# Kernel optimization log

Measured on AMD Instinct MI355X. Metric: run time of the kernel, lower is better.

Reference implementation:

```python
import jax, jax.numpy as jnp
import numpy as np

DIM = 1024
NUM_HEADS = 16
HEAD_DIM = 64
NUM_LANDMARKS = 256
SEQ_LEN = 4096
BATCH = 4


def setup_inputs() -> dict:
    key = jax.random.key(0)
    ks = jax.random.split(key, 10)
    hd = NUM_HEADS * HEAD_DIM
    s = 1.0 / np.sqrt(DIM)
    inp = {
        "X": jax.random.normal(ks[0], (BATCH, SEQ_LEN, DIM), jnp.float32),
        "mask": jnp.ones((BATCH, SEQ_LEN), jnp.float32),
        "Wq": jax.random.normal(ks[1], (DIM, hd), jnp.float32) * s,
        "bq": jnp.zeros((hd,), jnp.float32),
        "Wk": jax.random.normal(ks[2], (DIM, hd), jnp.float32) * s,
        "bk": jnp.zeros((hd,), jnp.float32),
        "Wv": jax.random.normal(ks[3], (DIM, hd), jnp.float32) * s,
        "bv": jnp.zeros((hd,), jnp.float32),
        "Wff": jax.random.normal(ks[4], (hd, DIM), jnp.float32) * (1.0 / np.sqrt(hd)),
        "bff": jnp.zeros((DIM,), jnp.float32),
    }
    return inp


def _iterative_inv(mat, n_iter=6):
    # mat: [B,H,m,m]; Newton-Schulz style pseudo-inverse, faithful to torch code
    m = mat.shape[-1]
    I = jnp.eye(m, dtype=mat.dtype)
    K = mat
    # global max over the whole tensor, as torch.max with no dim
    denom = jnp.max(jnp.sum(jnp.abs(K), axis=-2)) * jnp.max(jnp.sum(jnp.abs(K), axis=-1))
    V = jnp.swapaxes(K, -1, -2) / denom
    for _ in range(n_iter):
        KV = K @ V
        V = 0.25 * V @ (13.0 * I - KV @ (15.0 * I - KV @ (7.0 * I - KV)))
    return V


def _nystrom_attn(Q, K, V, mask):
    # Q,K,V: [B,H,S,D]; mask: [B,S]
    B, H, S, D = Q.shape
    m = NUM_LANDMARKS
    scale = np.sqrt(np.sqrt(HEAD_DIM)).astype(np.float32)
    Q = Q * mask[:, None, :, None] / scale
    K = K * mask[:, None, :, None] / scale
    Ql = Q.reshape(B, H, m, S // m, D).mean(axis=-2)  # [B,H,m,D]
    Kl = K.reshape(B, H, m, S // m, D).mean(axis=-2)
    k1 = jax.nn.softmax(jnp.einsum('bhsd,bhmd->bhsm', Q, Kl), axis=-1)   # [B,H,S,m]
    k2 = jax.nn.softmax(jnp.einsum('bhmd,bhnd->bhmn', Ql, Kl), axis=-1)  # [B,H,m,m]
    k3 = jax.nn.softmax(
        jnp.einsum('bhmd,bhsd->bhms', Ql, K) - 1e9 * (1.0 - mask[:, None, None, :]),
        axis=-1)  # [B,H,m,S]
    return k1 @ (_iterative_inv(k2) @ (k3 @ V))  # [B,H,S,D]


def reference(X, mask, Wq, bq, Wk, bk, Wv, bv, Wff, bff):
    B, S, _ = X.shape
    def split(t):  # [B,S,H*D] -> [B,H,S,D]
        return t.reshape(B, S, NUM_HEADS, HEAD_DIM).transpose(0, 2, 1, 3)
    Q = split(X @ Wq + bq)
    K = split(X @ Wk + bk)
    V = split(X @ Wv + bv)
    attn = _nystrom_attn(Q, K, V, mask)
    attn = attn.transpose(0, 2, 1, 3).reshape(B, S, NUM_HEADS * HEAD_DIM)
    return attn @ Wff + bff
```

## Files before the change

kernel.cpp:

```cpp
#include <hip/hip_runtime.h>
#include <cstdint>
#include <cstddef>


typedef unsigned short u16;
typedef __attribute__((ext_vector_type(8))) short short8;
typedef __attribute__((ext_vector_type(4))) float f32x4;
typedef __attribute__((ext_vector_type(4))) unsigned short us4;
typedef __attribute__((ext_vector_type(8))) unsigned short us8;

__device__ __forceinline__ float bf2f(u16 u){ return __uint_as_float(((unsigned int)u)<<16); }
__device__ __forceinline__ u16 f2bf(float x){
  unsigned int i = __float_as_uint(x);
  unsigned int r = i + 0x7FFFu + ((i>>16)&1u);
  return (u16)(r>>16);
}
__device__ __forceinline__ f32x4 mfma16(short8 a, short8 b, f32x4 c){
  return __builtin_amdgcn_mfma_f32_16x16x32_bf16(a,b,c,0,0,0);
}
__device__ __forceinline__ void gld16(const void* g, void* l){
  __builtin_amdgcn_global_load_lds(
      (const __attribute__((address_space(1))) unsigned int*)g,
      (__attribute__((address_space(3))) unsigned int*)l, 16, 0, 0);
}

template<typename T>
__device__ __forceinline__ void load4v(const T* p, float x[4]){
  if constexpr (sizeof(T)==4){
    f32x4 v = *(const f32x4*)p;
    #pragma unroll
    for (int c=0;c<4;c++) x[c]=v[c];
  } else {
    us4 v = *(const us4*)p;
    #pragma unroll
    for (int c=0;c<4;c++) x[c]=bf2f(v[c]);
  }
}

template<int BM,int BN,int AM,int AN,bool BTB,bool SPLIT,bool FUSESM,
         typename TA,typename TB,typename TC>
__global__ __launch_bounds__(256) void gemm_k(
    const TA* __restrict__ A, const TB* __restrict__ B, TC* __restrict__ C,
    int M, int N, int K,
    long long sA, long long sB, long long sC, int ldc)
{
  constexpr int WR = BM/(16*AM);
  constexpr int WC = BN/(16*AN);
  static_assert(WR*WC==4, "need 4 waves");
  constexpr int LDW = 40;
  constexpr int NROW = BM+BN;
  constexpr int LOFF = NROW*LDW;
  __shared__ u16 lds[(SPLIT?2:1)*NROW*LDW];

  const int tid = threadIdx.x;
  const int z = blockIdx.z;
  const TA* __restrict__ Az = A + (size_t)z*sA;
  const TB* __restrict__ Bz = B + (size_t)z*sB;
  TC* __restrict__ Cz = C + (size_t)z*sC;
  const int tileM = blockIdx.x*BM;
  const int tileN = blockIdx.y*BN;

  const int lane = tid & 63;
  const int wv   = tid >> 6;
  const int wr   = wv / WC;
  const int wc   = wv % WC;
  const int lrow = lane & 15;
  const int kgrp = lane >> 4;
  const int koff = kgrp*8;

  f32x4 acc[AM][AN];
  #pragma unroll
  for (int i=0;i<AM;i++)
    #pragma unroll
    for (int j=0;j<AN;j++)
      acc[i][j] = (f32x4){0.f,0.f,0.f,0.f};

  u16* ldsA = lds;
  u16* ldsB = lds + BM*LDW;

  const int nkt = K >> 5;
  for (int kt=0; kt<nkt; ++kt){
    const int k0 = kt << 5;
    #pragma unroll
    for (int s2=0; s2<BM/32; ++s2){
      int slot = tid + s2*256;
      int row = slot >> 3;
      int kc  = (slot & 7) << 2;
      float x[4];
      load4v(Az + (size_t)(tileM+row)*K + (k0+kc), x);
      us4 h, l;
      #pragma unroll
      for (int c=0;c<4;c++){
        h[c] = f2bf(x[c]);
        if constexpr (SPLIT) l[c] = f2bf(x[c] - bf2f(h[c]));
      }
      *(us4*)&ldsA[row*LDW + kc] = h;
      if constexpr (SPLIT) *(us4*)&ldsA[LOFF + row*LDW + kc] = l;
    }
    {
      #pragma unroll
      for (int s2=0; s2<BN/32; ++s2){
        int slot = tid + s2*256;
        int row = slot >> 3;
        int kc  = (slot & 7) << 2;
        float x[4];
        load4v(Bz + (size_t)(tileN+row)*K + (k0+kc), x);
        us4 h, l;
        #pragma unroll
        for (int c=0;c<4;c++){
          h[c] = f2bf(x[c]);
          if constexpr (SPLIT) l[c] = f2bf(x[c] - bf2f(h[c]));
        }
        *(us4*)&ldsB[row*LDW + kc] = h;
        if constexpr (SPLIT) *(us4*)&ldsB[LOFF + row*LDW + kc] = l;
      }
    }
    __syncthreads();
    short8 ah[AM], al[AM];
    #pragma unroll
    for (int i=0;i<AM;i++){
      ah[i] = *(const short8*)&ldsA[(wr*AM*16 + i*16 + lrow)*LDW + koff];
      if constexpr (SPLIT) al[i] = *(const short8*)&ldsA[LOFF + (wr*AM*16 + i*16 + lrow)*LDW + koff];
    }
    #pragma unroll
    for (int j=0;j<AN;j++){
      short8 bh = *(const short8*)&ldsB[(wc*AN*16 + j*16 + lrow)*LDW + koff];
      if constexpr (SPLIT){
        short8 bl = *(const short8*)&ldsB[LOFF + (wc*AN*16 + j*16 + lrow)*LDW + koff];
        #pragma unroll
        for (int i=0;i<AM;i++){
          acc[i][j] = mfma16(ah[i], bh, acc[i][j]);
          acc[i][j] = mfma16(ah[i], bl, acc[i][j]);
          acc[i][j] = mfma16(al[i], bh, acc[i][j]);
        }
      } else {
        #pragma unroll
        for (int i=0;i<AM;i++)
          acc[i][j] = mfma16(ah[i], bh, acc[i][j]);
      }
    }
    __syncthreads();
  }

  #pragma unroll
  for (int r=0;r<4;r++){
    float mx = -3.0e38f;
    #pragma unroll
    for (int j=0;j<AN;j++) mx = fmaxf(mx, acc[0][j][r]);
    #pragma unroll
    for (int d=1; d<16; d<<=1) mx = fmaxf(mx, __shfl_xor(mx, d));
    float p[AN]; float ss = 0.f;
    #pragma unroll
    for (int j=0;j<AN;j++){ p[j] = expf(acc[0][j][r]-mx); ss += p[j]; }
    #pragma unroll
    for (int d=1; d<16; d<<=1) ss += __shfl_xor(ss, d);
    float inv = 1.0f/ss;
    int row = tileM + wr*16 + kgrp*4 + r;
    #pragma unroll
    for (int j=0;j<AN;j++){
      int col = j*16 + lrow;
      Cz[(size_t)row*ldc + col] = p[j]*inv;
    }
  }
}

template<int OUT>
__global__ __launch_bounds__(256) void sgemm_k(
    const u16* __restrict__ Ah, const u16* __restrict__ Al,
    const u16* __restrict__ Bh, const u16* __restrict__ Bl,
    int K, long long sA, long long sB,
    u16* __restrict__ RoH, u16* __restrict__ RoL,
    u16* __restrict__ CoH, u16* __restrict__ CoL,
    float* __restrict__ Fo, long long sO, int ldO,
    float addI, float csgn, float scale,
    const float* __restrict__ bias, const float* __restrict__ ml)
{
  __shared__ u16 lds[16384];
  const int tid = threadIdx.x;
  const int z = blockIdx.z;
  const int tileM = blockIdx.x*64, tileN = blockIdx.y*64;
  const int lane = tid&63, wv = tid>>6;
  const int wr = wv>>1, wc = wv&1;
  const int lrow = lane&15, kgrp = lane>>4;

  const u16* __restrict__ base[4] = {
    Ah + (size_t)z*sA + (size_t)tileM*K,
    Al + (size_t)z*sA + (size_t)tileM*K,
    Bh + (size_t)z*sB + (size_t)tileN*K,
    Bl + (size_t)z*sB + (size_t)tileN*K };

  f32x4 acc[2][2];
  #pragma unroll
  for (int i=0;i<2;i++)
    #pragma unroll
    for (int j=0;j<2;j++) acc[i][j] = (f32x4){0.f,0.f,0.f,0.f};

  for (int k0=0; k0<K; k0+=64){
    #pragma unroll
    for (int t4=0; t4<4; ++t4){
      #pragma unroll
      for (int hf=0; hf<2; ++hf){
        int w = hf*256 + tid;
        int row = w>>3, c = w&7;
        int cs = c ^ (row&7);
        gld16(base[t4] + (size_t)row*K + k0 + cs*8, lds + t4*4096 + (w & ~63)*8);
      }
    }
    __syncthreads();
    #pragma unroll
    for (int kk=0; kk<2; ++kk){
      int ch = kk*4 + kgrp;
      short8 a_h[2], a_l[2], b_h[2], b_l[2];
      #pragma unroll
      for (int i=0;i<2;i++){
        int r = wr*32 + i*16 + lrow;
        int off = r*64 + ((ch ^ (r&7))<<3);
        a_h[i] = *(const short8*)&lds[off];
        a_l[i] = *(const short8*)&lds[4096 + off];
      }
      #pragma unroll
      for (int j=0;j<2;j++){
        int r = wc*32 + j*16 + lrow;
        int off = r*64 + ((ch ^ (r&7))<<3);
        b_h[j] = *(const short8*)&lds[8192 + off];
        b_l[j] = *(const short8*)&lds[12288 + off];
      }
      #pragma unroll
      for (int i=0;i<2;i++)
        #pragma unroll
        for (int j=0;j<2;j++){
          acc[i][j] = mfma16(a_h[i], b_h[j], acc[i][j]);
          acc[i][j] = mfma16(a_h[i], b_l[j], acc[i][j]);
          acc[i][j] = mfma16(a_l[i], b_h[j], acc[i][j]);
        }
    }
    __syncthreads();
  }

  if constexpr (OUT==0 || OUT==1){
    #pragma unroll
    for (int i=0;i<2;i++)
      #pragma unroll
      for (int j=0;j<2;j++){
        int rl0 = wr*32 + i*16 + kgrp*4;
        int cl  = wc*32 + j*16 + lrow;
        #pragma unroll
        for (int q=0;q<4;q++){
          int rl = rl0 + q;
          float p = acc[i][j][q]*scale;
          if constexpr (OUT==0){
            if (RoH){
              u16 h = f2bf(p);
              int lo = rl*64 + (cl ^ ((rl&7)<<3));
              lds[lo] = h;
              lds[4096 + lo] = f2bf(p - bf2f(h));
            }
            float cv = csgn*p + (((tileM+rl)==(tileN+cl))? addI : 0.f);
            u16 ch = f2bf(cv);
            int lo2 = cl*64 + (rl ^ ((cl&7)<<3));
            lds[8192 + lo2] = ch;
            lds[12288 + lo2] = f2bf(cv - bf2f(ch));
          } else {
            lds[cl*64 + (rl ^ ((cl&7)<<3))] = f2bf(p);
          }
        }
      }
    __syncthreads();
    if constexpr (OUT==0){
      if (RoH){
        #pragma unroll
        for (int c2=0;c2<2;c2++){
          int idx = c2*256 + tid;
          int row = idx>>3, seg = idx&7;
          int lo = row*64 + ((seg ^ (row&7))<<3);
          size_t go = (size_t)z*65536 + (size_t)(tileM+row)*256 + tileN + seg*8;
          *(us8*)&RoH[go] = *(const us8*)&lds[lo];
          *(us8*)&RoL[go] = *(const us8*)&lds[4096 + lo];
        }
      }
      #pragma unroll
      for (int c2=0;c2<2;c2++){
        int idx = c2*256 + tid;
        int row = idx>>3, seg = idx&7;
        int lo = row*64 + ((seg ^ (row&7))<<3);
        size_t go = (size_t)z*65536 + (size_t)(tileN+row)*256 + tileM + seg*8;
        *(us8*)&CoH[go] = *(const us8*)&lds[8192 + lo];
        *(us8*)&CoL[go] = *(const us8*)&lds[12288 + lo];
      }
    } else {
      #pragma unroll
      for (int c2=0;c2<2;c2++){
        int idx = c2*256 + tid;
        int row = idx>>3, seg = idx&7;
        int lo = row*64 + ((seg ^ (row&7))<<3);
        *(us8*)&CoH[(size_t)z*16384 + (size_t)(tileN+row)*256 + tileM + seg*8] =
            *(const us8*)&lds[lo];
      }
    }
  } else {
    #pragma unroll
    for (int i=0;i<2;i++)
      #pragma unroll
      for (int j=0;j<2;j++){
        int grow0 = tileM + wr*32 + i*16 + kgrp*4;
        int gcol  = tileN + wc*32 + j*16 + lrow;
        #pragma unroll
        for (int q=0;q<4;q++){
          int grow = grow0+q;
          float v = acc[i][j][q] + ml[grow]*bias[gcol];
          int b = grow>>8, l = grow&255, h = gcol>>6, d = gcol&63;
          size_t oi = (((size_t)(b*16+h)*256 + l)*64 + d);
          Fo[oi] = v;
          if (RoH) RoH[oi] = f2bf(v);
        }
      }
  }
}

template<int EPI>
__global__ __launch_bounds__(256) void fgemm_k(
    const u16* __restrict__ A, const u16* __restrict__ Bt, float* __restrict__ Cf,
    u16* __restrict__ Q_, u16* __restrict__ K_, u16* __restrict__ V_,
    int M, int N, int K, int nTilesN,
    const float* __restrict__ bias, const float* __restrict__ rowscale)
{
  __shared__ u16 lds[2*128*64];
  u16* ldsA = lds;
  u16* ldsB = lds + 128*64;

  int flat = blockIdx.y*nTilesN + blockIdx.x;
  int nwg  = gridDim.x*gridDim.y;
  int chunk = nwg >> 3;
  int nid = (flat & 7)*chunk + (flat >> 3);
  int bxM = nid / nTilesN, byN = nid % nTilesN;
  const int tileM = bxM*128, tileN = byN*128;

  const int tid = threadIdx.x;
  const int lane = tid & 63, wv = tid>>6;
  const int wr = wv>>1, wc = wv&1;
  const int lrow = lane&15, kgrp = lane>>4;

  f32x4 acc[4][4];
  #pragma unroll
  for (int i=0;i<4;i++)
    #pragma unroll
    for (int j=0;j<4;j++) acc[i][j] = (f32x4){0.f,0.f,0.f,0.f};

  for (int k0=0; k0<K; k0+=64){
    #pragma unroll
    for (int i=0;i<4;i++){
      int s = i*256 + tid;
      int row = s>>3, c = s&7;
      int cs = c ^ (row&7);
      gld16(A + (size_t)(tileM+row)*K + k0 + cs*8, ldsA + (size_t)(s & ~63)*8);
    }
    #pragma unroll
    for (int i=0;i<4;i++){
      int s = i*256 + tid;
      int row = s>>3, c = s&7;
      int cs = c ^ (row&7);
      gld16(Bt + (size_t)(tileN+row)*K + k0 + cs*8, ldsB + (size_t)(s & ~63)*8);
    }
    __syncthreads();
    #pragma unroll
    for (int kk=0; kk<2; ++kk){
      int ch = kk*4 + kgrp;
      short8 af[4], bf[4];
      #pragma unroll
      for (int i=0;i<4;i++){
        int r = wr*64 + i*16 + lrow;
        af[i] = *(const short8*)&ldsA[r*64 + ((ch^(r&7))<<3)];
      }
      #pragma unroll
      for (int j=0;j<4;j++){
        int r = wc*64 + j*16 + lrow;
        bf[j] = *(const short8*)&ldsB[r*64 + ((ch^(r&7))<<3)];
      }
      #pragma unroll
      for (int i=0;i<4;i++)
        #pragma unroll
        for (int j=0;j<4;j++)
          acc[i][j] = mfma16(af[i], bf[j], acc[i][j]);
    }
    __syncthreads();
  }

  if constexpr (EPI==0){
    #pragma unroll
    for (int i=0;i<4;i++)
      #pragma unroll
      for (int j=0;j<4;j++)
        #pragma unroll
        for (int q=0;q<4;q++){
          int row = tileM + wr*64 + i*16 + kgrp*4 + q;
          int col = tileN + wc*64 + j*16 + lrow;
          Cf[(size_t)row*N + col] = acc[i][j][q] + (bias ? bias[col] : 0.f);
        }
  } else {
    #pragma unroll
    for (int i=0;i<4;i++)
      #pragma unroll
      for (int j=0;j<4;j++)
        #pragma unroll
        for (int q=0;q<4;q++){
          int rloc = wr*64 + i*16 + kgrp*4 + q;
          int cloc = wc*64 + j*16 + lrow;
          int col = tileN + cloc;
          float v = acc[i][j][q] + bias[col];
          if ((col>>10) < 2) v *= rowscale[tileM + rloc];
          lds[rloc*128 + cloc] = f2bf(v);
        }
    __syncthreads();
    #pragma unroll
    for (int c=0;c<8;c++){
      int idx = c*256 + tid;
      int row = idx >> 4;
      int seg = idx & 15;
      int col = tileN + seg*8;
      int which = col >> 10;
      int hd = col & 1023, h = hd>>6, d0 = hd&63;
      int grow = tileM + row;
      int b = grow>>12, s = grow&4095;
      u16* dst = (which==0) ? Q_ : (which==1) ? K_ : V_;
      us8 v = *(const us8*)&lds[row*128 + seg*8];
      *(us8*)&dst[(((size_t)(b*16+h))*4096 + s)*64 + d0] = v;
    }
  }
}

__global__ __launch_bounds__(256) void o3p_k(
    const float* __restrict__ Ql, const u16* __restrict__ Kb, const u16* __restrict__ Vb,
    const float* __restrict__ mask, float* __restrict__ Opart, float* __restrict__ MLpart)
{
  constexpr int QHI=0, QLO=4096, KT=8192, VT=12288, PHI=16640, PLO=20736;
  __shared__ u16 lds[24832];
  const int bx = blockIdx.x, ck = blockIdx.y, z = blockIdx.z;
  const int tid = threadIdx.x;
  const int lane = tid&63, wv = tid>>6;
  const int lrow = lane&15, kgrp = lane>>4;
  const float* Qlz = Ql + (size_t)z*16384 + (size_t)bx*64*64;
  const u16* Kz = Kb + (size_t)z*4096*64;
  const u16* Vz = Vb + (size_t)z*4096*64;
  const float* mrow = mask + (size_t)(z>>4)*4096;

  #pragma unroll
  for (int i=0;i<2;i++){
    int s = i*256 + tid;
    int row = s>>3, c = s&7;
    const float* src = Qlz + row*64 + c*8;
    f32x4 v0 = *(const f32x4*)src;
    f32x4 v1 = *(const f32x4*)(src+4);
    us8 hi, lo;
    #pragma unroll
    for (int e=0;e<4;e++){
      hi[e] = f2bf(v0[e]); lo[e] = f2bf(v0[e]-bf2f(hi[e]));
      hi[4+e] = f2bf(v1[e]); lo[4+e] = f2bf(v1[e]-bf2f(hi[4+e]));
    }
    int ad = row*64 + ((c^(row&7))<<3);
    *(us8*)&lds[QHI+ad] = hi;
    *(us8*)&lds[QLO+ad] = lo;
  }

  float m_r[4], l_r[4];
  f32x4 oacc[4];
  #pragma unroll
  for (int r=0;r<4;r++){ m_r[r] = -3.0e38f; l_r[r] = 0.f; }
  #pragma unroll
  for (int j=0;j<4;j++) oacc[j] = (f32x4){0.f,0.f,0.f,0.f};

  for (int st=0; st<16; ++st){
    int s0 = (ck*16 + st)*64;
    #pragma unroll
    for (int i=0;i<2;i++){
      int s = i*256 + tid;
      int row = s>>3, c = s&7;
      int cs = c ^ (row&7);
      gld16(Kz + (size_t)(s0+row)*64 + cs*8, &lds[KT + (size_t)(s & ~63)*8]);
    }
    #pragma unroll
    for (int i=0;i<2;i++){
      int s = i*256 + tid;
      int row = s>>3, c = s&7;
      us8 v = *(const us8*)(Vz + (size_t)(s0+row)*64 + c*8);
      #pragma unroll
      for (int e=0;e<8;e++) lds[VT + (c*8+e)*68 + row] = v[e];
    }
    __syncthreads();

    f32x4 sacc[4];
    #pragma unroll
    for (int j=0;j<4;j++) sacc[j] = (f32x4){0.f,0.f,0.f,0.f};
    int qr = wv*16 + lrow;
    #pragma unroll
    for (int kk=0; kk<2; ++kk){
      int ch = kk*4 + kgrp;
      short8 ah = *(const short8*)&lds[QHI + qr*64 + ((ch^(qr&7))<<3)];
      short8 alo = *(const short8*)&lds[QLO + qr*64 + ((ch^(qr&7))<<3)];
      #pragma unroll
      for (int j=0;j<4;j++){
        int kr = j*16 + lrow;
        short8 bk = *(const short8*)&lds[KT + kr*64 + ((ch^(kr&7))<<3)];
        sacc[j] = mfma16(ah, bk, sacc[j]);
        sacc[j] = mfma16(alo, bk, sacc[j]);
      }
    }
    float mb[4];
    #pragma unroll
    for (int j=0;j<4;j++) mb[j] = -1.0e9f*(1.0f - mrow[s0 + j*16 + lrow]);
    #pragma unroll
    for (int j=0;j<4;j++)
      #pragma unroll
      for (int r=0;r<4;r++) sacc[j][r] += mb[j];

    #pragma unroll
    for (int r=0;r<4;r++){
      float tm = fmaxf(fmaxf(sacc[0][r],sacc[1][r]), fmaxf(sacc[2][r],sacc[3][r]));
      #pragma unroll
      for (int d=1; d<16; d<<=1) tm = fmaxf(tm, __shfl_xor(tm, d));
      float mn = fmaxf(m_r[r], tm);
      float scf = expf(m_r[r] - mn);
      float ps[4]; float tsum = 0.f;
      #pragma unroll
      for (int j=0;j<4;j++){ ps[j] = expf(sacc[j][r] - mn); tsum += ps[j]; }
      #pragma unroll
      for (int d=1; d<16; d<<=1) tsum += __shfl_xor(tsum, d);
      l_r[r] = l_r[r]*scf + tsum;
      m_r[r] = mn;
      #pragma unroll
      for (int j=0;j<4;j++) oacc[j][r] *= scf;
      int prow = kgrp*4 + r;
      #pragma unroll
      for (int j=0;j<4;j++){
        int key = j*16 + lrow;
        u16 phi = f2bf(ps[j]);
        u16 plo = f2bf(ps[j] - bf2f(phi));
        int ad = wv*1024 + prow*64 + (((key>>3)^(prow&7))<<3) + (key&7);
        lds[PHI+ad] = phi;
        lds[PLO+ad] = plo;
      }
    }

    #pragma unroll
    for (int kk=0; kk<2; ++kk){
      int ch = kk*4 + kgrp;
      int pr = lrow;
      short8 pah = *(const short8*)&lds[PHI + wv*1024 + pr*64 + ((ch^(pr&7))<<3)];
      short8 plo = *(const short8*)&lds[PLO + wv*1024 + pr*64 + ((ch^(pr&7))<<3)];
      #pragma unroll
      for (int j=0;j<4;j++){
        int vr = j*16 + lrow;
        int a0 = VT + vr*68 + ch*8;
        us4 p0 = *(const us4*)&lds[a0];
        us4 p1 = *(const us4*)&lds[a0+4];
        short8 bv_;
        #pragma unroll
        for (int e=0;e<4;e++){ bv_[e] = (short)p0[e]; bv_[4+e] = (short)p1[e]; }
        oacc[j] = mfma16(pah, bv_, oacc[j]);
        oacc[j] = mfma16(plo, bv_, oacc[j]);
      }
    }
    __syncthreads();
  }

  #pragma unroll
  for (int j=0;j<4;j++)
    #pragma unroll
    for (int r=0;r<4;r++){
      int rowl = bx*64 + wv*16 + kgrp*4 + r;
      Opart[(((size_t)(ck*64+z)*256 + rowl)*64) + j*16 + lrow] = oacc[j][r];
    }
  #pragma unroll
  for (int r=0;r<4;r++){
    if (lrow==0){
      int rowl = bx*64 + wv*16 + kgrp*4 + r;
      MLpart[((size_t)(ck*64+z)*256 + rowl)*2 + 0] = m_r[r];
      MLpart[((size_t)(ck*64+z)*256 + rowl)*2 + 1] = l_r[r];
    }
  }
}

__global__ __launch_bounds__(256) void o3c_k(const float* __restrict__ Opart,
    const float* __restrict__ MLpart, u16* __restrict__ O3Th, u16* __restrict__ O3Tl)
{
  int z = blockIdx.x; int t = threadIdx.x;
  float m[4], l[4];
  #pragma unroll
  for (int c=0;c<4;c++){
    m[c] = MLpart[((size_t)(c*64+z)*256 + t)*2 + 0];
    l[c] = MLpart[((size_t)(c*64+z)*256 + t)*2 + 1];
  }
  float M = fmaxf(fmaxf(m[0],m[1]), fmaxf(m[2],m[3]));
  float w[4]; float L = 0.f;
  #pragma unroll
  for (int c=0;c<4;c++){ w[c] = expf(m[c]-M); L += l[c]*w[c]; }
  float inv = 1.0f/L;
  for (int d0=0; d0<16; ++d0){
    f32x4 o = (f32x4){0.f,0.f,0.f,0.f};
    #pragma unroll
    for (int c=0;c<4;c++){
      f32x4 x = *(const f32x4*)(Opart + ((size_t)(c*64+z)*256 + t)*64 + d0*4);
      #pragma unroll
      for (int e=0;e<4;e++) o[e] += w[c]*x[e];
    }
    #pragma unroll
    for (int e=0;e<4;e++){
      float val = o[e]*inv;
      int d = d0*4+e;
      u16 h = f2bf(val);
      O3Th[((size_t)z*64 + d)*256 + t] = h;
      O3Tl[((size_t)z*64 + d)*256 + t] = f2bf(val - bf2f(h));
    }
  }
}

__global__ void fill_k(float* __restrict__ p, int n, float v){
  for (int i = blockIdx.x*256 + threadIdx.x; i < n; i += gridDim.x*256) p[i] = v;
}
__global__ void prep_k(const float* __restrict__ mask, float* __restrict__ rs,
                       const float* __restrict__ bq, const float* __restrict__ bk,
                       const float* __restrict__ bv, float* __restrict__ bqkv,
                       float* __restrict__ mx){
  int b = blockIdx.x;
  if (b < 64){
    int i = b*256 + threadIdx.x;
    rs[i] = mask[i] * 0.3535533905932738f;
  } else if (b < 76){
    int j = (b-64)*256 + threadIdx.x;
    bqkv[j] = (j<1024) ? bq[j] : (j<2048) ? bk[j-1024] : bv[j-2048];
  } else {
    if (threadIdx.x < 2) mx[threadIdx.x] = 0.f;
  }
}
__global__ __launch_bounds__(256) void wtr4_k(
    const float* __restrict__ Wq, const float* __restrict__ Wk,
    const float* __restrict__ Wv, const float* __restrict__ Wff,
    u16* __restrict__ Tqkv, u16* __restrict__ Tff){
  __shared__ float t[64][65];
  int zi = blockIdx.z;
  const float* W = (zi==0)?Wq:(zi==1)?Wk:(zi==2)?Wv:Wff;
  u16* T = (zi==3)? Tff : (Tqkv + (size_t)zi*1048576);
  int ti = blockIdx.x, tj = blockIdx.y;
  int tt = threadIdx.x; int c = tt&63, r0 = tt>>6;
  #pragma unroll
  for (int rr=0; rr<16; rr++){
    int r = rr*4 + r0;
    t[r][c] = W[(size_t)(ti*64+r)*1024 + tj*64 + c];
  }
  __syncthreads();
  #pragma unroll
  for (int rr=0; rr<16; rr++){
    int r = rr*4 + r0;
    T[(size_t)(tj*64 + r)*1024 + ti*64 + c] = f2bf(t[c][r]);
  }
}
__global__ __launch_bounds__(256) void wtrsplit2_k(
    const float* __restrict__ Wq, const float* __restrict__ Wk,
    u16* __restrict__ QH, u16* __restrict__ QL,
    u16* __restrict__ KH, u16* __restrict__ KL){
  __shared__ float t[64][65];
  int zi = blockIdx.z;
  const float* W = zi ? Wk : Wq;
  u16* TH = zi ? KH : QH;
  u16* TL = zi ? KL : QL;
  int ti = blockIdx.x, tj = blockIdx.y;
  int tt = threadIdx.x; int c = tt&63, r0 = tt>>6;
  #pragma unroll
  for (int rr=0; rr<16; rr++){
    int r = rr*4 + r0;
    t[r][c] = W[(size_t)(ti*64+r)*1024 + tj*64 + c];
  }
  __syncthreads();
  #pragma unroll
  for (int rr=0; rr<16; rr++){
    int r = rr*4 + r0;
    float v = t[c][r];
    u16 h = f2bf(v);
    TH[(size_t)(tj*64 + r)*1024 + ti*64 + c] = h;
    TL[(size_t)(tj*64 + r)*1024 + ti*64 + c] = f2bf(v - bf2f(h));
  }
}
__global__ __launch_bounds__(256) void pool_k(const float* __restrict__ X, const float* __restrict__ mask,
                                              u16* __restrict__ Xlh, u16* __restrict__ Xll,
                                              float* __restrict__ ml, u16* __restrict__ Xb){
  int bl = blockIdx.x; int b = bl>>8; int l = bl&255;
  const float* Xp = X + ((size_t)b*4096 + (size_t)l*16)*1024;
  const float* mp = mask + (size_t)b*4096 + (size_t)l*16;
  int t = threadIdx.x;
  f32x4 acc = (f32x4){0.f,0.f,0.f,0.f};
  float msum = 0.f;
  #pragma unroll
  for (int j=0;j<16;j++){
    float mj = mp[j];
    msum += mj;
    f32x4 x = *(const f32x4*)(Xp + (size_t)j*1024 + t*4);
    us4 xb;
    #pragma unroll
    for (int c=0;c<4;c++){ acc[c] += mj*x[c]; xb[c] = f2bf(x[c]); }
    *(us4*)(Xb + ((size_t)bl*16 + j)*1024 + t*4) = xb;
  }
  const float c0 = 0.02209708691207961f;
  us4 h, lo;
  #pragma unroll
  for (int c=0;c<4;c++){
    float v = acc[c]*c0;
    h[c] = f2bf(v);
    lo[c] = f2bf(v - bf2f(h[c]));
  }
  *(us4*)(Xlh + (size_t)bl*1024 + t*4) = h;
  *(us4*)(Xll + (size_t)bl*1024 + t*4) = lo;
  if (t==0) ml[bl] = msum * c0;
}
__global__ __launch_bounds__(256) void absmax_k(const float* __restrict__ k2, float* __restrict__ mx){
  int z = blockIdx.x; int t = threadIdx.x;
  const float* A = k2 + (size_t)z*65536;
  float rsum=0.f, csum=0.f;
  for (int j=0;j<256;j++){
    rsum += fabsf(A[t*256+j]);
    csum += fabsf(A[j*256+t]);
  }
  #pragma unroll
  for (int d=1; d<64; d<<=1){
    rsum = fmaxf(rsum, __shfl_xor(rsum, d));
    csum = fmaxf(csum, __shfl_xor(csum, d));
  }
  __shared__ float red[8];
  int wv=t>>6, ln=t&63;
  if (ln==0){ red[wv]=rsum; red[4+wv]=csum; }
  __syncthreads();
  if (t==0){
    float mr = fmaxf(fmaxf(red[0],red[1]),fmaxf(red[2],red[3]));
    float mc = fmaxf(fmaxf(red[4],red[5]),fmaxf(red[6],red[7]));
    atomicMax((int*)&mx[0], __float_as_int(mr));
    atomicMax((int*)&mx[1], __float_as_int(mc));
  }
}
__global__ __launch_bounds__(256) void v0prep_k(const float* __restrict__ K2f, const float* __restrict__ mx,
    u16* __restrict__ K2h, u16* __restrict__ K2l,
    u16* __restrict__ V0rh, u16* __restrict__ V0rl,
    u16* __restrict__ V0ch, u16* __restrict__ V0cl)
{
  int z = blockIdx.y; int bx = blockIdx.x;
  int ti = bx>>2, tj = bx&3;
  __shared__ float tile[64][65];
  const float* A = K2f + (size_t)z*65536;
  int t = threadIdx.x; int c = t&63, r0 = t>>6;
  float invden = 1.0f/(mx[0]*mx[1]);
  #pragma unroll
  for (int rr=0; rr<16; rr++){
    int r = rr*4 + r0;
    float v = A[(size_t)(ti*64 + r)*256 + tj*64 + c];
    tile[r][c] = v;
    size_t idx = (size_t)z*65536 + (size_t)(ti*64+r)*256 + tj*64 + c;
    u16 h = f2bf(v);
    K2h[idx] = h; K2l[idx] = f2bf(v - bf2f(h));
    float w = v*invden;
    h = f2bf(w);
    V0ch[idx] = h; V0cl[idx] = f2bf(w - bf2f(h));
  }
  __syncthreads();
  #pragma unroll
  for (int rr=0; rr<16; rr++){
    int r = rr*4 + r0;
    float w = tile[c][r]*invden;
    size_t idx = (size_t)z*65536 + (size_t)(tj*64+r)*256 + ti*64 + c;
    u16 h = f2bf(w);
    V0rh[idx] = h; V0rl[idx] = f2bf(w - bf2f(h));
  }
}

__device__ __forceinline__ int swz64(int row,int k){
  return row*64 + (((((k>>3)&7) ^ (row&7)))<<3) + (k&7);
}
__device__ __forceinline__ int swz256(int row,int k){
  return row*256 + ((((k>>3) ^ (row&7)))<<3) + (k&7);
}
__global__ __launch_bounds__(256) void attn_k(const u16* __restrict__ Qb,
    const u16* __restrict__ Klb, const u16* __restrict__ tTb,
    u16* __restrict__ attn){
  __shared__ u16 lds[32768];
  const int z = blockIdx.y;
  const int rows0 = blockIdx.x * 64;
  const int tid = threadIdx.x;
  const int lane = tid & 63, wv = tid>>6;
  const int lrow = lane & 15, kgrp = lane>>4;
  const u16* Qz = Qb + ((size_t)z*4096 + rows0)*64;
  const u16* Klz = Klb + (size_t)z*16384;
  const u16* tTz = tTb + (size_t)z*16384;

  #pragma unroll
  for (int i=0;i<8;i++){
    int s = i*256 + tid;
    int row = s>>3, c = s&7;
    gld16(Klz + (size_t)row*64 + ((c^(row&7))<<3), lds + (s & ~63)*8);
  }
  #pragma unroll
  for (int i=0;i<2;i++){
    int s = i*256 + tid;
    int row = s>>3, c = s&7;
    gld16(Qz + (size_t)row*64 + ((c^(row&7))<<3), lds + 16384 + (s & ~63)*8);
  }
  __syncthreads();

  f32x4 acc[4][4];
  #pragma unroll
  for (int i=0;i<4;i++)
    #pragma unroll
    for (int j=0;j<4;j++) acc[i][j] = (f32x4){0.f,0.f,0.f,0.f};
  #pragma unroll
  for (int ks=0; ks<2; ++ks){
    int ko = ks*32 + kgrp*8;
    short8 a[4], b[4];
    #pragma unroll
    for (int i=0;i<4;i++) a[i] = *(const short8*)&lds[16384 + swz64(16*i+lrow, ko)];
    #pragma unroll
    for (int j=0;j<4;j++) b[j] = *(const short8*)&lds[swz64(wv*64 + j*16 + lrow, ko)];
    #pragma unroll
    for (int i=0;i<4;i++)
      #pragma unroll
      for (int j=0;j<4;j++) acc[i][j] = mfma16(a[i], b[j], acc[i][j]);
  }
  __syncthreads();

  #pragma unroll
  for (int i=0;i<8;i++){
    int s = i*256 + tid;
    int row = s>>5, c = s&31;
    int gch = (c & ~7) | ((c ^ row) & 7);
    gld16(tTz + (size_t)row*256 + (gch<<3), lds + 16384 + (s & ~63)*8);
  }

  float* r0 = (float*)lds;
  float* r1 = r0 + 256;
  #pragma unroll
  for (int i=0;i<4;i++)
    #pragma unroll
    for (int r=0;r<4;r++){
      float mx = fmaxf(fmaxf(acc[i][0][r], acc[i][1][r]), fmaxf(acc[i][2][r], acc[i][3][r]));
      #pragma unroll
      for (int d=1; d<16; d<<=1) mx = fmaxf(mx, __shfl_xor(mx, d));
      if (lrow==0) r0[(16*i + kgrp*4 + r)*4 + wv] = mx;
    }
  __syncthreads();
  float inv_ir[4][4];
  #pragma unroll
  for (int i=0;i<4;i++)
    #pragma unroll
    for (int r=0;r<4;r++){
      int row = 16*i + kgrp*4 + r;
      float gm = fmaxf(fmaxf(r0[row*4+0], r0[row*4+1]), fmaxf(r0[row*4+2], r0[row*4+3]));
      float s = 0.f;
      #pragma unroll
      for (int j=0;j<4;j++){
        acc[i][j][r] = expf(acc[i][j][r] - gm);
        s += acc[i][j][r];
      }
      #pragma unroll
      for (int d=1; d<16; d<<=1) s += __shfl_xor(s, d);
      if (lrow==0) r1[row*4 + wv] = s;
      inv_ir[i][r] = 0.f; (void)inv_ir;
    }
  __syncthreads();
  #pragma unroll
  for (int i=0;i<4;i++)
    #pragma unroll
    for (int r=0;r<4;r++){
      int row = 16*i + kgrp*4 + r;
      inv_ir[i][r] = 1.0f/(r1[row*4+0]+r1[row*4+1]+r1[row*4+2]+r1[row*4+3]);
    }
  __syncthreads();

  #pragma unroll
  for (int i=0;i<4;i++)
    #pragma unroll
    for (int j=0;j<4;j++)
      #pragma unroll
      for (int r=0;r<4;r++){
        int row = 16*i + kgrp*4 + r;
        int l = wv*64 + j*16 + lrow;
        lds[swz256(row, l)] = f2bf(acc[i][j][r]*inv_ir[i][r]);
      }
  __syncthreads();

  f32x4 o[4];
  #pragma unroll
  for (int j=0;j<4;j++) o[j] = (f32x4){0.f,0.f,0.f,0.f};
  #pragma unroll
  for (int ks=0; ks<8; ++ks){
    int ko = ks*32 + kgrp*8;
    short8 a = *(const short8*)&lds[swz256(16*wv + lrow, ko)];
    #pragma unroll
    for (int j=0;j<4;j++){
      short8 bb = *(const short8*)&lds[16384 + swz256(j*16 + lrow, ko)];
      o[j] = mfma16(a, bb, o[j]);
    }
  }
  __syncthreads();
  #pragma unroll
  for (int j=0;j<4;j++)
    #pragma unroll
    for (int r=0;r<4;r++){
      int m = 16*wv + kgrp*4 + r;
      lds[m*64 + j*16 + lrow] = f2bf(o[j][r]);
    }
  __syncthreads();
  int b = z>>4, h = z&15;
  #pragma unroll
  for (int c=0;c<2;c++){
    int idx = c*256 + tid;
    int row = idx >> 3;
    int seg = idx & 7;
    us8 v = *(const us8*)&lds[row*64 + seg*8];
    *(us8*)&attn[((size_t)b*4096 + rows0 + row)*1024 + (size_t)h*64 + seg*8] = v;
  }
}

extern "C" void kernel_launch(void* const* d_in, const int* in_sizes, int n_in,
                              void* d_out, int out_size, void* d_ws, size_t ws_size,
                              hipStream_t stream) {
  (void)in_sizes; (void)n_in;
  const float* X    = (const float*)d_in[0];
  const float* mask = (const float*)d_in[1];
  const float* Wq   = (const float*)d_in[2];
  const float* bq   = (const float*)d_in[3];
  const float* Wk   = (const float*)d_in[4];
  const float* bk   = (const float*)d_in[5];
  const float* Wv   = (const float*)d_in[6];
  const float* bv   = (const float*)d_in[7];
  const float* Wff  = (const float*)d_in[8];
  const float* bff  = (const float*)d_in[9];
  float* outp = (float*)d_out;
  char* ws = (char*)d_ws;

  auto MiB = [](size_t x){ return x<<20; };
  const size_t O_QB   = 0;
  const size_t O_KB   = MiB(32);
  const size_t O_VB   = MiB(64);
  const size_t O_XB   = MiB(96);
  const size_t O_RG[4][2] = {
    {MiB(32),MiB(40)}, {MiB(48),MiB(56)}, {MiB(64),MiB(72)}, {MiB(80),MiB(88)} };
  const size_t O_OPART= MiB(96);
  const size_t O_MLP  = MiB(112);
  const size_t O_XAH  = MiB(96),  O_XAL = MiB(104);
  const size_t O_K2H  = MiB(112), O_K2L = MiB(120);
  const size_t O_K2F  = MiB(128);
  const size_t O_WQKVT= MiB(128);
  const size_t O_XLH  = MiB(134), O_XLL = MiB(136);
  const size_t O_WQTH = MiB(138), O_WQTL = MiB(140);
  const size_t O_QL   = MiB(144);
  const size_t O_TTB  = MiB(144);
  const size_t O_KL   = MiB(148);
  const size_t O_O3TH = MiB(152), O_O3TL = MiB(154);
  const size_t O_WKTH = MiB(152), O_WKTL = MiB(154);
  const size_t O_WFFT = MiB(156);
  const size_t O_KLB  = MiB(158);
  const size_t O_ATTN = MiB(32);
  const size_t O_RS   = MiB(162);
  const size_t O_ML   = O_RS + 65536;
  const size_t O_MX   = O_ML + 4096;
  const size_t O_BQKV = O_MX + 256;
  const size_t NEED   = O_BQKV + 16384;

  if (ws_size < NEED){
    fill_k<<<2048,256,0,stream>>>(outp, out_size, 1.0e9f);
    return;
  }

  u16*   Qb   = (u16*)(ws + O_QB);
  u16*   Kb   = (u16*)(ws + O_KB);
  u16*   Vb   = (u16*)(ws + O_VB);
  u16*   Xb   = (u16*)(ws + O_XB);
  u16*   WqkvT= (u16*)(ws + O_WQKVT);
  u16*   WffT = (u16*)(ws + O_WFFT);
  float* bqkv = (float*)(ws + O_BQKV);
  float* Ql   = (float*)(ws + O_QL);
  float* Kl   = (float*)(ws + O_KL);
  u16*   Klb  = (u16*)(ws + O_KLB);
  u16*   tTb  = (u16*)(ws + O_TTB);
  float* K2f  = (float*)(ws + O_K2F);
  float* rs   = (float*)(ws + O_RS);
  float* ml   = (float*)(ws + O_ML);
  float* Mx   = (float*)(ws + O_MX);
  float* Opart= (float*)(ws + O_OPART);
  float* MLp  = (float*)(ws + O_MLP);
  u16*   O3Th = (u16*)(ws + O_O3TH);
  u16*   O3Tl = (u16*)(ws + O_O3TL);
  u16*   K2h  = (u16*)(ws + O_K2H);
  u16*   K2l  = (u16*)(ws + O_K2L);
  u16*   XAh  = (u16*)(ws + O_XAH);
  u16*   XAl  = (u16*)(ws + O_XAL);
  u16*   Xlh  = (u16*)(ws + O_XLH);
  u16*   Xll  = (u16*)(ws + O_XLL);
  u16*   WqTh = (u16*)(ws + O_WQTH);
  u16*   WqTl = (u16*)(ws + O_WQTL);
  u16*   WkTh = (u16*)(ws + O_WKTH);
  u16*   WkTl = (u16*)(ws + O_WKTL);
  u16*   AttnB= (u16*)(ws + O_ATTN);
  u16* RGH[4]; u16* RGL[4];
  for (int i=0;i<4;i++){ RGH[i] = (u16*)(ws + O_RG[i][0]); RGL[i] = (u16*)(ws + O_RG[i][1]); }

  prep_k<<<77,256,0,stream>>>(mask, rs, bq, bk, bv, bqkv, Mx);
  pool_k<<<1024,256,0,stream>>>(X, mask, Xlh, Xll, ml, Xb);

  wtr4_k<<<dim3(16,16,4),256,0,stream>>>(Wq, Wk, Wv, Wff, WqkvT, WffT);
  fgemm_k<1><<<dim3(24,128),256,0,stream>>>(Xb, WqkvT, nullptr, Qb, Kb, Vb,
      16384, 3072, 1024, 24, bqkv, rs);

  wtrsplit2_k<<<dim3(16,16,2),256,0,stream>>>(Wq, Wk, WqTh, WqTl, WkTh, WkTl);
  sgemm_k<2><<<dim3(16,16,1),256,0,stream>>>(Xlh, Xll, WqTh, WqTl, 1024, 0, 0,
      nullptr,nullptr,nullptr,nullptr, Ql, 0, 0, 0.f, 0.f, 1.f, bq, ml);
  sgemm_k<2><<<dim3(16,16,1),256,0,stream>>>(Xlh, Xll, WkTh, WkTl, 1024, 0, 0,
      Klb,nullptr,nullptr,nullptr, Kl, 0, 0, 0.f, 0.f, 1.f, bk, ml);

  gemm_k<64,256,1,16,true,true,true,float,float,float><<<dim3(4,1,64),256,0,stream>>>(
      Ql, Kl, K2f, 256,256,64, 16384,16384,65536, 256);

  o3p_k<<<dim3(4,4,64),256,0,stream>>>(Ql, Kb, Vb, mask, Opart, MLp);
  o3c_k<<<64,256,0,stream>>>(Opart, MLp, O3Th, O3Tl);

  absmax_k<<<64,256,0,stream>>>(K2f, Mx);
  v0prep_k<<<dim3(16,64),256,0,stream>>>(K2f, Mx, K2h, K2l, RGH[1], RGL[1], RGH[0], RGL[0]);
  int vc=0, vr=1, kv=2, x2=3;
  for (int it=0; it<6; ++it){
    sgemm_k<0><<<dim3(4,4,64),256,0,stream>>>(K2h, K2l, RGH[vc], RGL[vc], 256, 65536, 65536,
        RGH[kv], RGL[kv], XAh, XAl, nullptr, 0, 0, 7.f, -1.f, 1.f, nullptr, nullptr);
    sgemm_k<0><<<dim3(4,4,64),256,0,stream>>>(RGH[kv], RGL[kv], XAh, XAl, 256, 65536, 65536,
        nullptr, nullptr, RGH[x2], RGL[x2], nullptr, 0, 0, 15.f, -1.f, 1.f, nullptr, nullptr);
    sgemm_k<0><<<dim3(4,4,64),256,0,stream>>>(RGH[kv], RGL[kv], RGH[x2], RGL[x2], 256, 65536, 65536,
        nullptr, nullptr, XAh, XAl, nullptr, 0, 0, 13.f, -1.f, 1.f, nullptr, nullptr);
    sgemm_k<0><<<dim3(4,4,64),256,0,stream>>>(RGH[vr], RGL[vr], XAh, XAl, 256, 65536, 65536,
        RGH[kv], RGL[kv], RGH[x2], RGL[x2], nullptr, 0, 0, 0.f, 1.f, 0.25f, nullptr, nullptr);
    int nvc=x2, nvr=kv, nkv=vc, nx2=vr;
    vc=nvc; vr=nvr; kv=nkv; x2=nx2;
  }
  sgemm_k<1><<<dim3(4,1,64),256,0,stream>>>(RGH[vr], RGL[vr], O3Th, O3Tl, 256, 65536, 16384,
      nullptr,nullptr, tTb, nullptr, nullptr, 0, 0, 0.f, 0.f, 1.f, nullptr, nullptr);

  attn_k<<<dim3(64,64),256,0,stream>>>(Qb, Klb, tTb, AttnB);

  fgemm_k<0><<<dim3(8,128),256,0,stream>>>(AttnB, WffT, outp, nullptr, nullptr, nullptr,
      16384, 1024, 1024, 8, bff, nullptr);
}
```

Before: 1.130 ms.

## Merge setup kernels and precompute bf16 hi/lo splits for landmark softmax GEMM

```diff
diff --git a/kernel.cpp b/kernel.cpp
--- a/kernel.cpp
+++ b/kernel.cpp
@@ -24,142 +24,84 @@
       (__attribute__((address_space(3))) unsigned int*)l, 16, 0, 0);
 }
 
-template<typename T>
-__device__ __forceinline__ void load4v(const T* p, float x[4]){
-  if constexpr (sizeof(T)==4){
-    f32x4 v = *(const f32x4*)p;
-    #pragma unroll
-    for (int c=0;c<4;c++) x[c]=v[c];
-  } else {
-    us4 v = *(const us4*)p;
-    #pragma unroll
-    for (int c=0;c<4;c++) x[c]=bf2f(v[c]);
-  }
-}
-
-template<int BM,int BN,int AM,int AN,bool BTB,bool SPLIT,bool FUSESM,
-         typename TA,typename TB,typename TC>
-__global__ __launch_bounds__(256) void gemm_k(
-    const TA* __restrict__ A, const TB* __restrict__ B, TC* __restrict__ C,
-    int M, int N, int K,
-    long long sA, long long sB, long long sC, int ldc)
+__global__ __launch_bounds__(256) void k2s_k(
+    const u16* __restrict__ Ah, const u16* __restrict__ Al,
+    const u16* __restrict__ Bh, const u16* __restrict__ Bl,
+    float* __restrict__ C)
 {
-  constexpr int WR = BM/(16*AM);
-  constexpr int WC = BN/(16*AN);
-  static_assert(WR*WC==4, "need 4 waves");
-  constexpr int LDW = 40;
-  constexpr int NROW = BM+BN;
-  constexpr int LOFF = NROW*LDW;
-  __shared__ u16 lds[(SPLIT?2:1)*NROW*LDW];
-
+  __shared__ u16 lds[40960];
   const int tid = threadIdx.x;
-  const int z = blockIdx.z;
-  const TA* __restrict__ Az = A + (size_t)z*sA;
-  const TB* __restrict__ Bz = B + (size_t)z*sB;
-  TC* __restrict__ Cz = C + (size_t)z*sC;
-  const int tileM = blockIdx.x*BM;
-  const int tileN = blockIdx.y*BN;
-
-  const int lane = tid & 63;
-  const int wv   = tid >> 6;
-  const int wr   = wv / WC;
-  const int wc   = wv % WC;
-  const int lrow = lane & 15;
-  const int kgrp = lane >> 4;
-  const int koff = kgrp*8;
-
-  f32x4 acc[AM][AN];
-  #pragma unroll
-  for (int i=0;i<AM;i++)
-    #pragma unroll
-    for (int j=0;j<AN;j++)
-      acc[i][j] = (f32x4){0.f,0.f,0.f,0.f};
-
-  u16* ldsA = lds;
-  u16* ldsB = lds + BM*LDW;
-
-  const int nkt = K >> 5;
-  for (int kt=0; kt<nkt; ++kt){
-    const int k0 = kt << 5;
-    #pragma unroll
-    for (int s2=0; s2<BM/32; ++s2){
-      int slot = tid + s2*256;
-      int row = slot >> 3;
-      int kc  = (slot & 7) << 2;
-      float x[4];
-      load4v(Az + (size_t)(tileM+row)*K + (k0+kc), x);
-      us4 h, l;
-      #pragma unroll
-      for (int c=0;c<4;c++){
-        h[c] = f2bf(x[c]);
-        if constexpr (SPLIT) l[c] = f2bf(x[c] - bf2f(h[c]));
-      }
-      *(us4*)&ldsA[row*LDW + kc] = h;
-      if constexpr (SPLIT) *(us4*)&ldsA[LOFF + row*LDW + kc] = l;
-    }
-    {
-      #pragma unroll
-      for (int s2=0; s2<BN/32; ++s2){
-        int slot = tid + s2*256;
-        int row = slot >> 3;
-        int kc  = (slot & 7) << 2;
-        float x[4];
-        load4v(Bz + (size_t)(tileN+row)*K + (k0+kc), x);
-        us4 h, l;
-        #pragma unroll
-        for (int c=0;c<4;c++){
-          h[c] = f2bf(x[c]);
-          if constexpr (SPLIT) l[c] = f2bf(x[c] - bf2f(h[c]));
-        }
-        *(us4*)&ldsB[row*LDW + kc] = h;
-        if constexpr (SPLIT) *(us4*)&ldsB[LOFF + row*LDW + kc] = l;
-      }
-    }
-    __syncthreads();
-    short8 ah[AM], al[AM];
-    #pragma unroll
-    for (int i=0;i<AM;i++){
-      ah[i] = *(const short8*)&ldsA[(wr*AM*16 + i*16 + lrow)*LDW + koff];
-      if constexpr (SPLIT) al[i] = *(const short8*)&ldsA[LOFF + (wr*AM*16 + i*16 + lrow)*LDW + koff];
-    }
-    #pragma unroll
-    for (int j=0;j<AN;j++){
-      short8 bh = *(const short8*)&ldsB[(wc*AN*16 + j*16 + lrow)*LDW + koff];
-      if constexpr (SPLIT){
-        short8 bl = *(const short8*)&ldsB[LOFF + (wc*AN*16 + j*16 + lrow)*LDW + koff];
-        #pragma unroll
-        for (int i=0;i<AM;i++){
-          acc[i][j] = mfma16(ah[i], bh, acc[i][j]);
-          acc[i][j] = mfma16(ah[i], bl, acc[i][j]);
-          acc[i][j] = mfma16(al[i], bh, acc[i][j]);
-        }
-      } else {
-        #pragma unroll
-        for (int i=0;i<AM;i++)
-          acc[i][j] = mfma16(ah[i], bh, acc[i][j]);
-      }
-    }
-    __syncthreads();
-  }
-
+  const int tileM = blockIdx.x*64;
+  const int z = blockIdx.y;
+  const int lane = tid&63, wv = tid>>6;
+  const int lrow = lane&15, kgrp = lane>>4;
+  const u16* baseAh = Ah + (size_t)z*16384 + (size_t)tileM*64;
+  const u16* baseAl = Al + (size_t)z*16384 + (size_t)tileM*64;
+  const u16* baseBh = Bh + (size_t)z*16384;
+  const u16* baseBl = Bl + (size_t)z*16384;
+
+  #pragma unroll
+  for (int it=0; it<2; ++it){
+    int w = it*256 + tid; int row = w>>3, c = w&7; int cs = c^(row&7);
+    gld16(baseAh + (size_t)row*64 + (cs<<3), lds + (w & ~63)*8);
+  }
+  #pragma unroll
+  for (int it=0; it<2; ++it){
+    int w = it*256 + tid; int row = w>>3, c = w&7; int cs = c^(row&7);
+    gld16(baseAl + (size_t)row*64 + (cs<<3), lds + 4096 + (w & ~63)*8);
+  }
+  #pragma unroll
+  for (int it=0; it<8; ++it){
+    int w = it*256 + tid; int row = w>>3, c = w&7; int cs = c^(row&7);
+    gld16(baseBh + (size_t)row*64 + (cs<<3), lds + 8192 + (w & ~63)*8);
+  }
+  #pragma unroll
+  for (int it=0; it<8; ++it){
+    int w = it*256 + tid; int row = w>>3, c = w&7; int cs = c^(row&7);
+    gld16(baseBl + (size_t)row*64 + (cs<<3), lds + 24576 + (w & ~63)*8);
+  }
+  __syncthreads();
+
+  f32x4 acc[16];
+  #pragma unroll
+  for (int j=0;j<16;j++) acc[j] = (f32x4){0.f,0.f,0.f,0.f};
+
+  #pragma unroll
+  for (int kt=0; kt<2; ++kt){
+    int ch = kt*4 + kgrp;
+    int ra = wv*16 + lrow;
+    short8 ah = *(const short8*)&lds[ra*64 + ((ch^(ra&7))<<3)];
+    short8 al = *(const short8*)&lds[4096 + ra*64 + ((ch^(ra&7))<<3)];
+    #pragma unroll
+    for (int j=0;j<16;j++){
+      int rb = j*16 + lrow;
+      short8 bh = *(const short8*)&lds[8192 + rb*64 + ((ch^(rb&7))<<3)];
+      short8 bl = *(const short8*)&lds[24576 + rb*64 + ((ch^(rb&7))<<3)];
+      acc[j] = mfma16(ah, bh, acc[j]);
+      acc[j] = mfma16(ah, bl, acc[j]);
+      acc[j] = mfma16(al, bh, acc[j]);
+    }
+  }
+
+  float* Cz = C + (size_t)z*65536;
   #pragma unroll
   for (int r=0;r<4;r++){
     float mx = -3.0e38f;
     #pragma unroll
-    for (int j=0;j<AN;j++) mx = fmaxf(mx, acc[0][j][r]);
+    for (int j=0;j<16;j++) mx = fmaxf(mx, acc[j][r]);
     #pragma unroll
     for (int d=1; d<16; d<<=1) mx = fmaxf(mx, __shfl_xor(mx, d));
-    float p[AN]; float ss = 0.f;
-    #pragma unroll
-    for (int j=0;j<AN;j++){ p[j] = expf(acc[0][j][r]-mx); ss += p[j]; }
+    float p[16]; float ss = 0.f;
+    #pragma unroll
+    for (int j=0;j<16;j++){ p[j] = expf(acc[j][r]-mx); ss += p[j]; }
     #pragma unroll
     for (int d=1; d<16; d<<=1) ss += __shfl_xor(ss, d);
     float inv = 1.0f/ss;
-    int row = tileM + wr*16 + kgrp*4 + r;
-    #pragma unroll
-    for (int j=0;j<AN;j++){
+    int row = tileM + wv*16 + kgrp*4 + r;
+    #pragma unroll
+    for (int j=0;j<16;j++){
       int col = j*16 + lrow;
-      Cz[(size_t)row*ldc + col] = p[j]*inv;
+      Cz[(size_t)row*256 + col] = p[j]*inv;
     }
   }
 }
@@ -311,7 +253,11 @@
           int b = grow>>8, l = grow&255, h = gcol>>6, d = gcol&63;
           size_t oi = (((size_t)(b*16+h)*256 + l)*64 + d);
           Fo[oi] = v;
-          if (RoH) RoH[oi] = f2bf(v);
+          if (RoH){
+            u16 hh = f2bf(v);
+            RoH[oi] = hh;
+            RoL[oi] = f2bf(v - bf2f(hh));
+          }
         }
       }
   }
@@ -616,67 +562,67 @@
 __global__ void fill_k(float* __restrict__ p, int n, float v){
   for (int i = blockIdx.x*256 + threadIdx.x; i < n; i += gridDim.x*256) p[i] = v;
 }
-__global__ void prep_k(const float* __restrict__ mask, float* __restrict__ rs,
-                       const float* __restrict__ bq, const float* __restrict__ bk,
-                       const float* __restrict__ bv, float* __restrict__ bqkv,
-                       float* __restrict__ mx){
-  int b = blockIdx.x;
-  if (b < 64){
-    int i = b*256 + threadIdx.x;
-    rs[i] = mask[i] * 0.3535533905932738f;
-  } else if (b < 76){
-    int j = (b-64)*256 + threadIdx.x;
-    bqkv[j] = (j<1024) ? bq[j] : (j<2048) ? bk[j-1024] : bv[j-2048];
-  } else {
-    if (threadIdx.x < 2) mx[threadIdx.x] = 0.f;
-  }
-}
-__global__ __launch_bounds__(256) void wtr4_k(
+__global__ __launch_bounds__(256) void setup_k(
+    const float* __restrict__ mask, float* __restrict__ rs,
+    const float* __restrict__ bq, const float* __restrict__ bk,
+    const float* __restrict__ bv, float* __restrict__ bqkv, float* __restrict__ mx,
     const float* __restrict__ Wq, const float* __restrict__ Wk,
     const float* __restrict__ Wv, const float* __restrict__ Wff,
-    u16* __restrict__ Tqkv, u16* __restrict__ Tff){
+    u16* __restrict__ Tqkv, u16* __restrict__ Tff,
+    u16* __restrict__ QH, u16* __restrict__ QL,
+    u16* __restrict__ KH, u16* __restrict__ KL)
+{
   __shared__ float t[64][65];
-  int zi = blockIdx.z;
-  const float* W = (zi==0)?Wq:(zi==1)?Wk:(zi==2)?Wv:Wff;
-  u16* T = (zi==3)? Tff : (Tqkv + (size_t)zi*1048576);
-  int ti = blockIdx.x, tj = blockIdx.y;
+  int b = blockIdx.x;
+  if (b < 77){
+    if (b < 64){
+      int i = b*256 + threadIdx.x;
+      rs[i] = mask[i] * 0.3535533905932738f;
+    } else if (b < 76){
+      int j = (b-64)*256 + threadIdx.x;
+      bqkv[j] = (j<1024) ? bq[j] : (j<2048) ? bk[j-1024] : bv[j-2048];
+    } else {
+      if (threadIdx.x < 2) mx[threadIdx.x] = 0.f;
+    }
+    return;
+  }
   int tt = threadIdx.x; int c = tt&63, r0 = tt>>6;
-  #pragma unroll
-  for (int rr=0; rr<16; rr++){
-    int r = rr*4 + r0;
-    t[r][c] = W[(size_t)(ti*64+r)*1024 + tj*64 + c];
-  }
-  __syncthreads();
-  #pragma unroll
-  for (int rr=0; rr<16; rr++){
-    int r = rr*4 + r0;
-    T[(size_t)(tj*64 + r)*1024 + ti*64 + c] = f2bf(t[c][r]);
-  }
-}
-__global__ __launch_bounds__(256) void wtrsplit2_k(
-    const float* __restrict__ Wq, const float* __restrict__ Wk,
-    u16* __restrict__ QH, u16* __restrict__ QL,
-    u16* __restrict__ KH, u16* __restrict__ KL){
-  __shared__ float t[64][65];
-  int zi = blockIdx.z;
-  const float* W = zi ? Wk : Wq;
-  u16* TH = zi ? KH : QH;
-  u16* TL = zi ? KL : QL;
-  int ti = blockIdx.x, tj = blockIdx.y;
-  int tt = threadIdx.x; int c = tt&63, r0 = tt>>6;
-  #pragma unroll
-  for (int rr=0; rr<16; rr++){
-    int r = rr*4 + r0;
-    t[r][c] = W[(size_t)(ti*64+r)*1024 + tj*64 + c];
-  }
-  __syncthreads();
-  #pragma unroll
-  for (int rr=0; rr<16; rr++){
-    int r = rr*4 + r0;
-    float v = t[c][r];
-    u16 h = f2bf(v);
-    TH[(size_t)(tj*64 + r)*1024 + ti*64 + c] = h;
-    TL[(size_t)(tj*64 + r)*1024 + ti*64 + c] = f2bf(v - bf2f(h));
+  if (b < 77+1024){
+    int f = b - 77;
+    int zi = f >> 8; int r2 = f & 255; int ti = r2 & 15; int tj = r2 >> 4;
+    const float* W = (zi==0)?Wq:(zi==1)?Wk:(zi==2)?Wv:Wff;
+    u16* T = (zi==3)? Tff : (Tqkv + (size_t)zi*1048576);
+    #pragma unroll
+    for (int rr=0; rr<16; rr++){
+      int r = rr*4 + r0;
+      t[r][c] = W[(size_t)(ti*64+r)*1024 + tj*64 + c];
+    }
+    __syncthreads();
+    #pragma unroll
+    for (int rr=0; rr<16; rr++){
+      int r = rr*4 + r0;
+      T[(size_t)(tj*64 + r)*1024 + ti*64 + c] = f2bf(t[c][r]);
+    }
+  } else {
+    int f = b - 77 - 1024;
+    int zi = f >> 8; int r2 = f & 255; int ti = r2 & 15; int tj = r2 >> 4;
+    const float* W = zi ? Wk : Wq;
+    u16* TH = zi ? KH : QH;
+    u16* TL = zi ? KL : QL;
+    #pragma unroll
+    for (int rr=0; rr<16; rr++){
+      int r = rr*4 + r0;
+      t[r][c] = W[(size_t)(ti*64+r)*1024 + tj*64 + c];
+    }
+    __syncthreads();
+    #pragma unroll
+    for (int rr=0; rr<16; rr++){
+      int r = rr*4 + r0;
+      float v = t[c][r];
+      u16 h = f2bf(v);
+      TH[(size_t)(tj*64 + r)*1024 + ti*64 + c] = h;
+      TL[(size_t)(tj*64 + r)*1024 + ti*64 + c] = f2bf(v - bf2f(h));
+    }
   }
 }
 __global__ __launch_bounds__(256) void pool_k(const float* __restrict__ X, const float* __restrict__ mask,
@@ -938,6 +884,7 @@
   const size_t O_XB   = MiB(96);
   const size_t O_RG[4][2] = {
     {MiB(32),MiB(40)}, {MiB(48),MiB(56)}, {MiB(64),MiB(72)}, {MiB(80),MiB(88)} };
+  const size_t O_QLH  = MiB(96),  O_QLL = MiB(98), O_KLL = MiB(100);
   const size_t O_OPART= MiB(96);
   const size_t O_MLP  = MiB(112);
   const size_t O_XAH  = MiB(96),  O_XAL = MiB(104);
@@ -974,6 +921,9 @@
   float* bqkv = (float*)(ws + O_BQKV);
   float* Ql   = (float*)(ws + O_QL);
   float* Kl   = (float*)(ws + O_KL);
+  u16*   QlH  = (u16*)(ws + O_QLH);
+  u16*   QlL  = (u16*)(ws + O_QLL);
+  u16*   KlL  = (u16*)(ws + O_KLL);
   u16*   Klb  = (u16*)(ws + O_KLB);
   u16*   tTb  = (u16*)(ws + O_TTB);
   float* K2f  = (float*)(ws + O_K2F);
@@ -998,21 +948,19 @@
   u16* RGH[4]; u16* RGL[4];
   for (int i=0;i<4;i++){ RGH[i] = (u16*)(ws + O_RG[i][0]); RGL[i] = (u16*)(ws + O_RG[i][1]); }
 
-  prep_k<<<77,256,0,stream>>>(mask, rs, bq, bk, bv, bqkv, Mx);
+  setup_k<<<1613,256,0,stream>>>(mask, rs, bq, bk, bv, bqkv, Mx,
+      Wq, Wk, Wv, Wff, WqkvT, WffT, WqTh, WqTl, WkTh, WkTl);
   pool_k<<<1024,256,0,stream>>>(X, mask, Xlh, Xll, ml, Xb);
 
-  wtr4_k<<<dim3(16,16,4),256,0,stream>>>(Wq, Wk, Wv, Wff, WqkvT, WffT);
   fgemm_k<1><<<dim3(24,128),256,0,stream>>>(Xb, WqkvT, nullptr, Qb, Kb, Vb,
       16384, 3072, 1024, 24, bqkv, rs);
 
-  wtrsplit2_k<<<dim3(16,16,2),256,0,stream>>>(Wq, Wk, WqTh, WqTl, WkTh, WkTl);
   sgemm_k<2><<<dim3(16,16,1),256,0,stream>>>(Xlh, Xll, WqTh, WqTl, 1024, 0, 0,
-      nullptr,nullptr,nullptr,nullptr, Ql, 0, 0, 0.f, 0.f, 1.f, bq, ml);
+      QlH, QlL, nullptr, nullptr, Ql, 0, 0, 0.f, 0.f, 1.f, bq, ml);
   sgemm_k<2><<<dim3(16,16,1),256,0,stream>>>(Xlh, Xll, WkTh, WkTl, 1024, 0, 0,
-      Klb,nullptr,nullptr,nullptr, Kl, 0, 0, 0.f, 0.f, 1.f, bk, ml);
-
-  gemm_k<64,256,1,16,true,true,true,float,float,float><<<dim3(4,1,64),256,0,stream>>>(
-      Ql, Kl, K2f, 256,256,64, 16384,16384,65536, 256);
+      Klb, KlL, nullptr, nullptr, Kl, 0, 0, 0.f, 0.f, 1.f, bk, ml);
+
+  k2s_k<<<dim3(4,64),256,0,stream>>>(QlH, QlL, Klb, KlL, K2f);
 
   o3p_k<<<dim3(4,4,64),256,0,stream>>>(Ql, Kb, Vb, mask, Opart, MLp);
   o3c_k<<<64,256,0,stream>>>(Opart, MLp, O3Th, O3Tl);
```

Measured after the change: 1.114 ms. About the same (-1.4%).
